# Optimization experiments

Hardware: AMD Instinct MI355X
Metric: run time of the kernel (lower is better)

Reference implementation:

```python
import jax, jax.numpy as jnp
import numpy as np

B, S, D, H = 2, 2048, 1024, 16
DK = D // H


def setup_inputs() -> dict:
    key = jax.random.key(0)
    ks = jax.random.split(key, 10)
    scale = 1.0 / np.sqrt(D)
    x = jax.random.normal(ks[0], (B, S, D), dtype=jnp.float32)
    # causal mask: 1 = attend, 0 = masked (module's create_causal_mask)
    mask = jnp.tril(jnp.ones((S, S), dtype=jnp.int32))[None, None]
    Wq = jax.random.normal(ks[1], (D, D), jnp.float32) * scale
    bq = jax.random.normal(ks[2], (D,), jnp.float32) * 0.01
    Wk = jax.random.normal(ks[3], (D, D), jnp.float32) * scale
    bk = jax.random.normal(ks[4], (D,), jnp.float32) * 0.01
    Wv = jax.random.normal(ks[5], (D, D), jnp.float32) * scale
    bv = jax.random.normal(ks[6], (D,), jnp.float32) * 0.01
    Wo = jax.random.normal(ks[7], (D, D), jnp.float32) * scale
    bo = jax.random.normal(ks[8], (D,), jnp.float32) * 0.01
    return {"x": x, "mask": mask, "Wq": Wq, "bq": bq, "Wk": Wk, "bk": bk,
            "Wv": Wv, "bv": bv, "Wo": Wo, "bo": bo}


def reference(x, mask, Wq, bq, Wk, bk, Wv, bv, Wo, bo):
    b, s, _ = x.shape
    # projections; [B,S,D] -> [B,H,S,DK]
    def split_heads(t):
        return t.reshape(b, s, H, DK).transpose(0, 2, 1, 3)
    Q = split_heads(x @ Wq + bq)
    K = split_heads(x @ Wk + bk)
    V = split_heads(x @ Wv + bv)
    scores = jnp.einsum('bhqd,bhkd->bhqk', Q, K) / np.sqrt(DK)
    scores = jnp.where(mask == 0, jnp.float32(-1e9), scores)
    attn = jax.nn.softmax(scores, axis=-1)  # dropout p=0 -> identity
    ctx = jnp.einsum('bhqk,bhkd->bhqd', attn, V)
    ctx = ctx.transpose(0, 2, 1, 3).reshape(b, s, D)
    return ctx @ Wo + bo
```

## Files before the change

### kernel.cpp

```cpp
#include <hip/hip_runtime.h>
#include <hip/hip_bf16.h>


typedef _Float16 f16x8 __attribute__((ext_vector_type(8)));
typedef _Float16 f16x4 __attribute__((ext_vector_type(4)));
typedef _Float16 f16x2 __attribute__((ext_vector_type(2)));
typedef float f32x4 __attribute__((ext_vector_type(4)));

#define QSCALE 0.180336880111112f

__device__ __forceinline__ void async_copy16(const _Float16* gsrc,
                                             _Float16* ldst) {
  __builtin_amdgcn_global_load_lds(
      (const __attribute__((address_space(1))) void*)gsrc,
      (__attribute__((address_space(3))) void*)ldst, 16, 0, 0);
}

__global__ __launch_bounds__(256) void prep(
    const float* __restrict__ x, _Float16* __restrict__ xh,
    const float* __restrict__ W0, const float* __restrict__ W1,
    const float* __restrict__ W2, const float* __restrict__ W3,
    _Float16* __restrict__ T0, _Float16* __restrict__ T1,
    _Float16* __restrict__ T2, _Float16* __restrict__ T3) {
  if (blockIdx.x < 4096) {
    int i = (blockIdx.x * 256 + threadIdx.x) * 4;
    float4 v = *(const float4*)(x + i);
    f16x4 o;
    o.x = (_Float16)v.x; o.y = (_Float16)v.y;
    o.z = (_Float16)v.z; o.w = (_Float16)v.w;
    *(f16x4*)(xh + i) = o;
    return;
  }
  const int id = blockIdx.x - 4096;
  const int w = id >> 10, rem = id & 1023;
  const int bx = rem & 31, by = rem >> 5;
  const float* W; _Float16* T;
  switch (w) {
    case 0: W = W0; T = T0; break;
    case 1: W = W1; T = T1; break;
    case 2: W = W2; T = T2; break;
    default: W = W3; T = T3; break;
  }
  __shared__ _Float16 tile[32][33];
  const int tx = threadIdx.x & 31, ty = threadIdx.x >> 5;
  const int n0 = bx * 32, k0 = by * 32;
  for (int i = 0; i < 4; i++) {
    int kk = k0 + ty + i * 8;
    tile[ty + i * 8][tx] = (_Float16)W[(size_t)kk * 1024 + n0 + tx];
  }
  __syncthreads();
  for (int i = 0; i < 4; i++) {
    int nn = n0 + ty + i * 8;
    T[(size_t)nn * 1024 + k0 + tx] = tile[tx][ty + i * 8];
  }
}

__global__ __launch_bounds__(256) void gemm_qkv(
    const _Float16* __restrict__ A, const _Float16* __restrict__ BtAll,
    const float* __restrict__ bq, const float* __restrict__ bk,
    const float* __restrict__ bv, _Float16* __restrict__ Qh,
    _Float16* __restrict__ Kh, _Float16* __restrict__ VT) {
  __shared__ _Float16 As[128 * 32];
  __shared__ _Float16 Bs[128 * 32];
  __shared__ _Float16 tbuf[64 * 136];
  const int tid = threadIdx.x;
  const int wave = tid >> 6, lane = tid & 63;
  const int lr = lane & 15, lq = lane >> 4;
  const int m0 = blockIdx.x * 128, n0 = blockIdx.y * 128;
  const int rw = (wave & 1) * 64, cw = (wave >> 1) * 64;

  const int sel = blockIdx.y >> 3;
  const float* bias = sel == 0 ? bq : (sel == 1 ? bk : bv);
  const int c0 = n0 & 1023;

  f32x4 acc[4][4] = {};
  const int r0 = wave * 32 + (lane >> 2);
  const int woff = (lane & 3) * 8;

  for (int kt = 0; kt < 1024; kt += 32) {
    __syncthreads();
    async_copy16(A + (size_t)(m0 + r0) * 1024 + kt + woff, As + r0 * 32 + woff);
    async_copy16(A + (size_t)(m0 + r0 + 16) * 1024 + kt + woff,
                 As + (r0 + 16) * 32 + woff);
    async_copy16(BtAll + (size_t)(n0 + r0) * 1024 + kt + woff,
                 Bs + r0 * 32 + woff);
    async_copy16(BtAll + (size_t)(n0 + r0 + 16) * 1024 + kt + woff,
                 Bs + (r0 + 16) * 32 + woff);
    __syncthreads();
    f16x8 af[4], bf[4];
    for (int i = 0; i < 4; i++)
      af[i] = *(const f16x8*)(As + (rw + i * 16 + lr) * 32 + lq * 8);
    for (int j = 0; j < 4; j++)
      bf[j] = *(const f16x8*)(Bs + (cw + j * 16 + lr) * 32 + lq * 8);
    for (int i = 0; i < 4; i++)
      for (int j = 0; j < 4; j++)
        acc[i][j] = __builtin_amdgcn_mfma_f32_16x16x32_f16(af[i], bf[j],
                                                           acc[i][j], 0, 0, 0);
  }

  if (sel == 2) {
    const int bb = m0 >> 11, ss0 = m0 & 2047;
    const int cs = tid & 15, dkr = tid >> 4;
    for (int jj = 0; jj < 2; jj++) {
      __syncthreads();
      if ((wave >> 1) == jj) {
        for (int i = 0; i < 4; i++) {
          const int sl = rw + i * 16 + lq * 4;
          for (int j = 0; j < 4; j++) {
            const int dk = j * 16 + lr;
            const float bvl = bias[c0 + jj * 64 + dk];
            f16x4 pv;
            for (int r = 0; r < 4; r++) pv[r] = (_Float16)(acc[i][j][r] + bvl);
            *(f16x4*)(tbuf + dk * 136 + sl) = pv;
          }
        }
      }
      __syncthreads();
      const int hh = (c0 + jj * 64) >> 6;
      _Float16* dst = VT + ((size_t)(bb * 16 + hh) * 64) * 2048 + ss0;
      for (int k = 0; k < 4; k++) {
        const int dk = dkr + k * 16;
        *(uint4*)(dst + (size_t)dk * 2048 + cs * 8) =
            *(const uint4*)(tbuf + dk * 136 + cs * 8);
      }
    }
  } else {
    _Float16* out = sel == 0 ? Qh : Kh;
    const float scl = sel == 0 ? QSCALE : 1.0f;
    for (int i = 0; i < 4; i++) {
      const int row = m0 + rw + i * 16 + lq * 4;
      for (int j = 0; j < 4; j++) {
        const int col = c0 + cw + j * 16 + lr;
        const float bvl = bias[col];
        for (int r = 0; r < 4; r++)
          out[(size_t)(row + r) * 1024 + col] =
              (_Float16)((acc[i][j][r] + bvl) * scl);
      }
    }
  }
}

__global__ __launch_bounds__(256) void gemm_out(
    const _Float16* __restrict__ A, const _Float16* __restrict__ Bt,
    const float* __restrict__ bias, float* __restrict__ out) {
  __shared__ _Float16 As[128 * 32];
  __shared__ _Float16 Bs[64 * 32];
  const int tid = threadIdx.x;
  const int wave = tid >> 6, lane = tid & 63;
  const int lr = lane & 15, lq = lane >> 4;
  const int m0 = blockIdx.x * 128, n0 = blockIdx.y * 64;
  const int rw = (wave & 1) * 64, cw = (wave >> 1) * 32;
  f32x4 acc[4][2] = {};
  const int r0 = wave * 32 + (lane >> 2);
  const int br = tid >> 2;
  const int woff = (lane & 3) * 8;

  for (int kt = 0; kt < 1024; kt += 32) {
    __syncthreads();
    async_copy16(A + (size_t)(m0 + r0) * 1024 + kt + woff, As + r0 * 32 + woff);
    async_copy16(A + (size_t)(m0 + r0 + 16) * 1024 + kt + woff,
                 As + (r0 + 16) * 32 + woff);
    async_copy16(Bt + (size_t)(n0 + br) * 1024 + kt + woff,
                 Bs + br * 32 + woff);
    __syncthreads();
    f16x8 af[4], bf[2];
    for (int i = 0; i < 4; i++)
      af[i] = *(const f16x8*)(As + (rw + i * 16 + lr) * 32 + lq * 8);
    for (int j = 0; j < 2; j++)
      bf[j] = *(const f16x8*)(Bs + (cw + j * 16 + lr) * 32 + lq * 8);
    for (int i = 0; i < 4; i++)
      for (int j = 0; j < 2; j++)
        acc[i][j] = __builtin_amdgcn_mfma_f32_16x16x32_f16(af[i], bf[j],
                                                           acc[i][j], 0, 0, 0);
  }
  for (int i = 0; i < 4; i++) {
    const int row = m0 + rw + i * 16 + lq * 4;
    for (int j = 0; j < 2; j++) {
      const int col = n0 + cw + j * 16 + lr;
      const float bvl = bias[col];
      for (int r = 0; r < 4; r++)
        out[(size_t)(row + r) * 1024 + col] = acc[i][j][r] + bvl;
    }
  }
}

__global__ __launch_bounds__(256) void attn(const _Float16* __restrict__ Q,
                                            const _Float16* __restrict__ K,
                                            const _Float16* __restrict__ VT,
                                            _Float16* __restrict__ ctx) {
  const int qy = blockIdx.y, li = qy & 7;
  int qt;
  switch (qy >> 3) {
    case 0: qt = 31 - li; break;
    case 1: qt = 16 + li; break;
    case 2: qt = 15 - li; break;
    default: qt = li; break;
  }
  const int bh = blockIdx.x;
  const int b = bh >> 4, h = bh & 15;
  const int tid = threadIdx.x, wave = tid >> 6, lane = tid & 63;
  const int lr = lane & 15, lq = lane >> 4;
  const int qmin = qt * 64 + wave * 16;
  const size_t qkbase = ((size_t)b * 2048) * 1024 + h * 64;
  const size_t vtbase = ((size_t)bh) * 64 * 2048;

  __shared__ _Float16 Ks[2][64 * 72];
  __shared__ _Float16 Vs[2][64 * 72];

  const _Float16* qp = Q + qkbase + (size_t)(qmin + lr) * 1024 + lq * 8;
  f16x8 qf0 = *(const f16x8*)qp;
  f16x8 qf1 = *(const f16x8*)(qp + 32);

  f16x4 onesf;
  {
    _Float16 ov = (lr == 0) ? (_Float16)1.0f : (_Float16)0.0f;
    for (int i = 0; i < 4; i++) onesf[i] = ov;
  }

  f32x4 o[4] = {};
  f32x4 ol = {};

  const int sgr = tid >> 2, sgc = (tid & 3) * 8;
  const _Float16* Kg0 = K + qkbase + (size_t)sgr * 1024 + sgc;
  const _Float16* Vg0 = VT + vtbase + (size_t)sgr * 2048 + sgc;
  uint4 ka = *(const uint4*)Kg0, kb = *(const uint4*)(Kg0 + 32);
  uint4 va = *(const uint4*)Vg0, vb = *(const uint4*)(Vg0 + 32);

  for (int t = 0; t <= qt; t++) {
    _Float16* ksb = Ks[t & 1];
    _Float16* vsb = Vs[t & 1];
    *(uint4*)(ksb + sgr * 72 + sgc) = ka;
    *(uint4*)(ksb + sgr * 72 + sgc + 32) = kb;
    *(uint4*)(vsb + sgr * 72 + sgc) = va;
    *(uint4*)(vsb + sgr * 72 + sgc + 32) = vb;
    __syncthreads();
    if (t < qt) {
      const _Float16* kg = Kg0 + (size_t)(t + 1) * 64 * 1024;
      const _Float16* vg = Vg0 + (t + 1) * 64;
      ka = *(const uint4*)kg; kb = *(const uint4*)(kg + 32);
      va = *(const uint4*)vg; vb = *(const uint4*)(vg + 32);
    }

    const int kv0 = t * 64;
    f32x4 s[4];
    for (int ks = 0; ks < 4; ks++) {
      f16x8 k0 = *(const f16x8*)(ksb + (ks * 16 + lr) * 72 + lq * 8);
      f16x8 k1 = *(const f16x8*)(ksb + (ks * 16 + lr) * 72 + 32 + lq * 8);
      f32x4 z = {};
      z = __builtin_amdgcn_mfma_f32_16x16x32_f16(k0, qf0, z, 0, 0, 0);
      z = __builtin_amdgcn_mfma_f32_16x16x32_f16(k1, qf1, z, 0, 0, 0);
      s[ks] = z;
    }
    if (t == qt) {
      const int qcol = qmin + lr;
      for (int ks = 0; ks < 4; ks++)
        for (int r = 0; r < 4; r++)
          if (kv0 + ks * 16 + lq * 4 + r > qcol) s[ks][r] = -1e30f;
    }
    f16x4 pa[4];
    for (int ks = 0; ks < 4; ks++) {
      float p0 = exp2f(s[ks][0]);
      float p1 = exp2f(s[ks][1]);
      float p2 = exp2f(s[ks][2]);
      float p3 = exp2f(s[ks][3]);
      f16x2 q01 = __builtin_bit_cast(f16x2, __builtin_amdgcn_cvt_pkrtz(p0, p1));
      f16x2 q23 = __builtin_bit_cast(f16x2, __builtin_amdgcn_cvt_pkrtz(p2, p3));
      pa[ks] = __builtin_shufflevector(q01, q23, 0, 1, 2, 3);
    }
    for (int ks = 0; ks < 4; ks++) {
      for (int dn = 0; dn < 4; dn++) {
        f16x4 vf =
            *(const f16x4*)(vsb + (dn * 16 + lr) * 72 + ks * 16 + lq * 4);
        o[dn] =
            __builtin_amdgcn_mfma_f32_16x16x16f16(pa[ks], vf, o[dn], 0, 0, 0);
      }
      ol = __builtin_amdgcn_mfma_f32_16x16x16f16(pa[ks], onesf, ol, 0, 0, 0);
    }
  }

  for (int r = 0; r < 4; r++) {
    float lv = __shfl(ol[r], lane & 48);
    float inv = 1.0f / lv;
    const int row = qmin + lq * 4 + r;
    for (int dn = 0; dn < 4; dn++)
      ctx[qkbase + (size_t)row * 1024 + dn * 16 + lr] =
          (_Float16)(o[dn][r] * inv);
  }
}

extern "C" void kernel_launch(void* const* d_in, const int* in_sizes, int n_in,
                              void* d_out, int out_size, void* d_ws,
                              size_t ws_size, hipStream_t stream) {
  const float* x  = (const float*)d_in[0];
  const float* Wq = (const float*)d_in[2];
  const float* bq = (const float*)d_in[3];
  const float* Wk = (const float*)d_in[4];
  const float* bk = (const float*)d_in[5];
  const float* Wv = (const float*)d_in[6];
  const float* bv = (const float*)d_in[7];
  const float* Wo = (const float*)d_in[8];
  const float* bo = (const float*)d_in[9];
  float* out = (float*)d_out;

  char* ws = (char*)d_ws;
  const size_t MB = 1 << 20;
  _Float16* xh  = (_Float16*)(ws);
  _Float16* WTs = (_Float16*)(ws + 8 * MB);
  _Float16* WqT = WTs;
  _Float16* WkT = (_Float16*)(ws + 10 * MB);
  _Float16* WvT = (_Float16*)(ws + 12 * MB);
  _Float16* WoT = (_Float16*)(ws + 14 * MB);
  _Float16* Qh  = (_Float16*)(ws + 16 * MB);
  _Float16* Kh  = (_Float16*)(ws + 24 * MB);
  _Float16* VT  = (_Float16*)(ws + 32 * MB);
  _Float16* ctx = (_Float16*)(ws);

  prep<<<8192, 256, 0, stream>>>(x, xh, Wq, Wk, Wv, Wo, WqT, WkT, WvT, WoT);
  gemm_qkv<<<dim3(32, 24), 256, 0, stream>>>(xh, WTs, bq, bk, bv, Qh, Kh, VT);
  attn<<<dim3(32, 32), 256, 0, stream>>>(Qh, Kh, VT, ctx);
  gemm_out<<<dim3(32, 16), 256, 0, stream>>>(ctx, WoT, bo, out);
}
```

Baseline: 191.6 us.

## Split long causal query tiles across two KV-range blocks and add a combine kernel

```diff
diff --git a/kernel.cpp b/kernel.cpp
--- a/kernel.cpp
+++ b/kernel.cpp
@@ -184,18 +184,27 @@
   }
 }
 
-__global__ __launch_bounds__(256) void attn(const _Float16* __restrict__ Q,
-                                            const _Float16* __restrict__ K,
-                                            const _Float16* __restrict__ VT,
-                                            _Float16* __restrict__ ctx) {
-  const int qy = blockIdx.y, li = qy & 7;
-  int qt;
-  switch (qy >> 3) {
-    case 0: qt = 31 - li; break;
-    case 1: qt = 16 + li; break;
-    case 2: qt = 15 - li; break;
-    default: qt = li; break;
-  }
+__global__ __launch_bounds__(256) void attn(
+    const _Float16* __restrict__ Q, const _Float16* __restrict__ K,
+    const _Float16* __restrict__ VT, _Float16* __restrict__ ctx,
+    _Float16* __restrict__ Ph1, float* __restrict__ Lbuf) {
+#define E(q, lo, hi) ((q) | ((lo) << 8) | ((hi) << 16))
+  static const unsigned int slots[48] = {
+      E(31, 0, 16),  E(30, 0, 16),  E(29, 15, 30), E(14, 0, 15),
+      E(13, 0, 14),  E(24, 0, 13),  E(23, 0, 12),  E(11, 0, 12),
+      E(31, 16, 32), E(15, 0, 16),  E(28, 0, 15),  E(27, 14, 28),
+      E(25, 0, 13),  E(12, 0, 13),  E(23, 12, 24), E(21, 0, 11),
+      E(30, 16, 31), E(29, 0, 15),  E(28, 15, 29), E(26, 0, 14),
+      E(25, 13, 26), E(24, 13, 25), E(22, 0, 12),  E(21, 11, 22),
+      E(18, 10, 19), E(17, 9, 18),  E(27, 0, 14),  E(26, 14, 27),
+      E(20, 11, 21), E(22, 12, 23), E(19, 0, 10),  E(20, 0, 11),
+      E(17, 0, 9),   E(16, 9, 17),  E(4, 0, 5),    E(5, 0, 6),
+      E(16, 0, 9),   E(8, 0, 9),    E(19, 10, 20), E(10, 0, 11),
+      E(0, 0, 1),    E(1, 0, 2),    E(2, 0, 3),    E(3, 0, 4),
+      E(6, 0, 7),    E(7, 0, 8),    E(9, 0, 10),   E(18, 0, 10)};
+#undef E
+  const unsigned int e = slots[blockIdx.y];
+  const int qt = e & 63, kvlo = (e >> 8) & 63, kvhi = (e >> 16) & 63;
   const int bh = blockIdx.x;
   const int b = bh >> 4, h = bh & 15;
   const int tid = threadIdx.x, wave = tid >> 6, lane = tid & 63;
@@ -204,8 +213,8 @@
   const size_t qkbase = ((size_t)b * 2048) * 1024 + h * 64;
   const size_t vtbase = ((size_t)bh) * 64 * 2048;
 
-  __shared__ _Float16 Ks[2][64 * 72];
-  __shared__ _Float16 Vs[2][64 * 72];
+  __shared__ _Float16 Ks[64 * 72];
+  __shared__ _Float16 Vs[64 * 72];
 
   const _Float16* qp = Q + qkbase + (size_t)(qmin + lr) * 1024 + lq * 8;
   f16x8 qf0 = *(const f16x8*)qp;
@@ -223,18 +232,18 @@
   const int sgr = tid >> 2, sgc = (tid & 3) * 8;
   const _Float16* Kg0 = K + qkbase + (size_t)sgr * 1024 + sgc;
   const _Float16* Vg0 = VT + vtbase + (size_t)sgr * 2048 + sgc;
-  uint4 ka = *(const uint4*)Kg0, kb = *(const uint4*)(Kg0 + 32);
-  uint4 va = *(const uint4*)Vg0, vb = *(const uint4*)(Vg0 + 32);
-
-  for (int t = 0; t <= qt; t++) {
-    _Float16* ksb = Ks[t & 1];
-    _Float16* vsb = Vs[t & 1];
-    *(uint4*)(ksb + sgr * 72 + sgc) = ka;
-    *(uint4*)(ksb + sgr * 72 + sgc + 32) = kb;
-    *(uint4*)(vsb + sgr * 72 + sgc) = va;
-    *(uint4*)(vsb + sgr * 72 + sgc + 32) = vb;
-    __syncthreads();
-    if (t < qt) {
+  uint4 ka = *(const uint4*)(Kg0 + (size_t)kvlo * 64 * 1024);
+  uint4 kb = *(const uint4*)(Kg0 + (size_t)kvlo * 64 * 1024 + 32);
+  uint4 va = *(const uint4*)(Vg0 + kvlo * 64);
+  uint4 vb = *(const uint4*)(Vg0 + kvlo * 64 + 32);
+
+  for (int t = kvlo; t < kvhi; t++) {
+    *(uint4*)(Ks + sgr * 72 + sgc) = ka;
+    *(uint4*)(Ks + sgr * 72 + sgc + 32) = kb;
+    *(uint4*)(Vs + sgr * 72 + sgc) = va;
+    *(uint4*)(Vs + sgr * 72 + sgc + 32) = vb;
+    __syncthreads();
+    if (t + 1 < kvhi) {
       const _Float16* kg = Kg0 + (size_t)(t + 1) * 64 * 1024;
       const _Float16* vg = Vg0 + (t + 1) * 64;
       ka = *(const uint4*)kg; kb = *(const uint4*)(kg + 32);
@@ -244,8 +253,8 @@
     const int kv0 = t * 64;
     f32x4 s[4];
     for (int ks = 0; ks < 4; ks++) {
-      f16x8 k0 = *(const f16x8*)(ksb + (ks * 16 + lr) * 72 + lq * 8);
-      f16x8 k1 = *(const f16x8*)(ksb + (ks * 16 + lr) * 72 + 32 + lq * 8);
+      f16x8 k0 = *(const f16x8*)(Ks + (ks * 16 + lr) * 72 + lq * 8);
+      f16x8 k1 = *(const f16x8*)(Ks + (ks * 16 + lr) * 72 + 32 + lq * 8);
       f32x4 z = {};
       z = __builtin_amdgcn_mfma_f32_16x16x32_f16(k0, qf0, z, 0, 0, 0);
       z = __builtin_amdgcn_mfma_f32_16x16x32_f16(k1, qf1, z, 0, 0, 0);
@@ -269,22 +278,66 @@
     }
     for (int ks = 0; ks < 4; ks++) {
       for (int dn = 0; dn < 4; dn++) {
-        f16x4 vf =
-            *(const f16x4*)(vsb + (dn * 16 + lr) * 72 + ks * 16 + lq * 4);
+        f16x4 vf = *(const f16x4*)(Vs + (dn * 16 + lr) * 72 + ks * 16 + lq * 4);
         o[dn] =
             __builtin_amdgcn_mfma_f32_16x16x16f16(pa[ks], vf, o[dn], 0, 0, 0);
       }
       ol = __builtin_amdgcn_mfma_f32_16x16x16f16(pa[ks], onesf, ol, 0, 0, 0);
     }
-  }
-
-  for (int r = 0; r < 4; r++) {
-    float lv = __shfl(ol[r], lane & 48);
-    float inv = 1.0f / lv;
-    const int row = qmin + lq * 4 + r;
-    for (int dn = 0; dn < 4; dn++)
-      ctx[qkbase + (size_t)row * 1024 + dn * 16 + lr] =
-          (_Float16)(o[dn][r] * inv);
+    __syncthreads();
+  }
+
+  if (qt < 16) {
+    for (int r = 0; r < 4; r++) {
+      float lv = __shfl(ol[r], lane & 48);
+      float inv = 1.0f / lv;
+      const int row = qmin + lq * 4 + r;
+      for (int dn = 0; dn < 4; dn++)
+        ctx[qkbase + (size_t)row * 1024 + dn * 16 + lr] =
+            (_Float16)(o[dn][r] * inv);
+    }
+  } else {
+    const int hh = kvlo ? 1 : 0;
+    const int qtz = qt - 16;
+    if (lr == 0) {
+      for (int r = 0; r < 4; r++)
+        Lbuf[((hh * 32 + bh) * 16 + qtz) * 64 + wave * 16 + lq * 4 + r] = ol[r];
+    }
+    for (int r = 0; r < 4; r++) {
+      const int lrow = wave * 16 + lq * 4 + r;
+      if (hh == 0) {
+        const int row = qmin + lq * 4 + r;
+        for (int dn = 0; dn < 4; dn++)
+          ctx[qkbase + (size_t)row * 1024 + dn * 16 + lr] =
+              (_Float16)o[dn][r];
+      } else {
+        _Float16* pp = Ph1 + ((size_t)(bh * 16 + qtz) * 64 + lrow) * 64;
+        for (int dn = 0; dn < 4; dn++)
+          pp[dn * 16 + lr] = (_Float16)o[dn][r];
+      }
+    }
+  }
+}
+
+__global__ __launch_bounds__(256) void combine(_Float16* __restrict__ ctx,
+                                               const _Float16* __restrict__ Ph1,
+                                               const float* __restrict__ Lbuf) {
+  const int qtz = blockIdx.x, bh = blockIdx.y;
+  const int b = bh >> 4, hd = bh & 15;
+  const int row = threadIdx.x >> 2, c0 = (threadIdx.x & 3) * 16;
+  const float l0 = Lbuf[((0 * 32 + bh) * 16 + qtz) * 64 + row];
+  const float l1 = Lbuf[((1 * 32 + bh) * 16 + qtz) * 64 + row];
+  const float inv = 1.0f / (l0 + l1);
+  const int s = (qtz + 16) * 64 + row;
+  _Float16* cp = ctx + ((size_t)(b * 2048 + s)) * 1024 + hd * 64 + c0;
+  const _Float16* pp = Ph1 + ((size_t)(bh * 16 + qtz) * 64 + row) * 64 + c0;
+  for (int v = 0; v < 2; v++) {
+    f16x8 a = *(const f16x8*)(cp + v * 8);
+    f16x8 bb = *(const f16x8*)(pp + v * 8);
+    f16x8 ov;
+    for (int i = 0; i < 8; i++)
+      ov[i] = (_Float16)(((float)a[i] + (float)bb[i]) * inv);
+    *(f16x8*)(cp + v * 8) = ov;
   }
 }
 
@@ -314,9 +367,12 @@
   _Float16* Kh  = (_Float16*)(ws + 24 * MB);
   _Float16* VT  = (_Float16*)(ws + 32 * MB);
   _Float16* ctx = (_Float16*)(ws);
+  _Float16* Ph1 = (_Float16*)(ws + 8 * MB);
+  float*    Lbf = (float*)(ws + 12 * MB);
 
   prep<<<8192, 256, 0, stream>>>(x, xh, Wq, Wk, Wv, Wo, WqT, WkT, WvT, WoT);
   gemm_qkv<<<dim3(32, 24), 256, 0, stream>>>(xh, WTs, bq, bk, bv, Qh, Kh, VT);
-  attn<<<dim3(32, 32), 256, 0, stream>>>(Qh, Kh, VT, ctx);
+  attn<<<dim3(32, 48), 256, 0, stream>>>(Qh, Kh, VT, ctx, Ph1, Lbf);
+  combine<<<dim3(16, 32), 256, 0, stream>>>(ctx, Ph1, Lbf);
   gemm_out<<<dim3(32, 16), 256, 0, stream>>>(ctx, WoT, bo, out);
 }
```

After: 203.0 us. 5.9% more time.
